# Kernel optimization log

Hardware: AMD Instinct MI355X
Metric: run time of the kernel (lower is better)

Reference implementation:

```python
import jax, jax.numpy as jnp
import numpy as np

N_NODES = 100000
N_EDGES = 1600000
MUL = 32            # channel multiplicity for every irrep
INV_SQRT_MUL = 1.0 / np.sqrt(32.0)
# path constants: wigner-3j norms (1/sqrt3 for 0x1->1 and 1x1->0, 1/sqrt6 for 1x1->1)
# combined with fan-in path normalization (fan=32 for 0e out, fan=64 for 1o out, 2 paths)
C_DOT = 1.0 / np.sqrt(3.0 * 32.0)
C_SCL = 1.0 / np.sqrt(3.0 * 64.0)
C_CRS = 1.0 / np.sqrt(6.0 * 64.0)


def setup_inputs() -> dict:
    key = jax.random.key(0)
    ks = jax.random.split(key, 12)
    x = jax.random.normal(ks[0], (N_NODES, 128), jnp.float32)
    pos = jax.random.normal(ks[1], (N_NODES, 3), jnp.float32)
    edge_index = jax.random.randint(ks[2], (2, N_EDGES), 0, N_NODES, jnp.int32)
    # o3.Linear(32x0e+32x1o -> 32x0e+32x0e+32x1o): per-irrep channel mixing
    W_node_s = jax.random.normal(ks[3], (32, 64), jnp.float32)   # 0e -> (scalars|gates)
    W_node_v = jax.random.normal(ks[4], (32, 32), jnp.float32)   # 1o -> 1o
    # FullyConnectedTensorProduct(32x0e+32x1o, 1x1o -> 32x0e+32x1o): 3 CG paths
    W_tp_d = jax.random.normal(ks[5], (32, 32), jnp.float32)     # 1o x 1o -> 0e (dot)
    W_tp_s = jax.random.normal(ks[6], (32, 32), jnp.float32)     # 0e x 1o -> 1o
    W_tp_c = jax.random.normal(ks[7], (32, 32), jnp.float32)     # 1o x 1o -> 1o (cross)
    # o3.Linear(32x0e+32x1o -> 32x0e+32x1o)
    W_msg_s = jax.random.normal(ks[8], (32, 32), jnp.float32)
    W_msg_v = jax.random.normal(ks[9], (32, 32), jnp.float32)
    ln_gamma = jnp.ones((128,), jnp.float32)
    ln_beta = jnp.zeros((128,), jnp.float32)
    return {"x": x, "pos": pos, "edge_index": edge_index,
            "W_node_s": W_node_s, "W_node_v": W_node_v,
            "W_tp_d": W_tp_d, "W_tp_s": W_tp_s, "W_tp_c": W_tp_c,
            "W_msg_s": W_msg_s, "W_msg_v": W_msg_v,
            "ln_gamma": ln_gamma, "ln_beta": ln_beta}


def reference(x, pos, edge_index, W_node_s, W_node_v, W_tp_d, W_tp_s, W_tp_c,
              W_msg_s, W_msg_v, ln_gamma, ln_beta):
    N = x.shape[0]
    row, col = edge_index[0], edge_index[1]
    # split node irreps: 32 scalars (0e) | 32 vectors (1o) of dim 3
    s = x[:, :32]                       # [N,32]
    v = x[:, 32:].reshape(-1, 32, 3)    # [N,32,3]
    # lin_node (equivariant linear, path-normalized by 1/sqrt(fan_in)=1/sqrt(32))
    h_s = (s @ W_node_s) * INV_SQRT_MUL                          # [N,64]
    h_v = jnp.einsum('nid,ij->njd', v, W_node_v) * INV_SQRT_MUL  # [N,32,3]
    # Gate: relu scalars, sigmoid gates multiply the gated vectors
    sc = jax.nn.relu(h_s[:, :32])                                # [N,32]
    hv = h_v * jax.nn.sigmoid(h_s[:, 32:])[:, :, None]           # [N,32,3]
    # spherical harmonics l=1, component norm: sqrt(3)*unit vec in e3nn (y,z,x) order
    rel = pos[col] - pos[row]                                    # [E,3]
    unit = rel / jnp.sqrt(jnp.sum(rel * rel, -1, keepdims=True) + 1e-12)
    u = jnp.sqrt(3.0) * unit[:, (1, 2, 0)]                       # [E,3]
    # gather source-node features per edge
    sj = sc[col]                                                 # [E,32]
    vj = hv[col]                                                 # [E,32,3]
    # CG tensor product paths
    dot = jnp.einsum('eid,ed->ei', vj, u)                        # 1o x 1o -> 0e
    crs = jnp.cross(vj, u[:, None, :])                           # 1o x 1o -> 1o
    m0 = (dot @ W_tp_d) * C_DOT                                  # [E,32]
    m1 = (sj @ W_tp_s)[:, :, None] * u[:, None, :] * C_SCL \
         + jnp.einsum('eid,ik->ekd', crs, W_tp_c) * C_CRS        # [E,32,3]
    m = jnp.concatenate([m0, m1.reshape(-1, 96)], -1)            # [E,128]
    # scatter-mean over destination nodes (row)
    deg = jax.ops.segment_sum(jnp.ones_like(row, jnp.float32), row,
                              num_segments=N).clip(1.0)
    mi = jax.ops.segment_sum(m, row, num_segments=N) / deg[:, None]
    # lin_msg
    ms = (mi[:, :32] @ W_msg_s) * INV_SQRT_MUL
    mv = jnp.einsum('nid,ij->njd', mi[:, 32:].reshape(-1, 32, 3),
                    W_msg_v) * INV_SQRT_MUL
    o = jnp.concatenate([ms, mv.reshape(-1, 96)], -1)            # [N,128]
    # LayerNorm over 128 dims (as in the original, affine)
    mu = o.mean(-1, keepdims=True)
    var = o.var(-1, keepdims=True)
    o = (o - mu) / jnp.sqrt(var + 1e-5) * ln_gamma + ln_beta
    return x + o
```

## Files before the change

### kernel.cpp

```cpp
#include <hip/hip_runtime.h>
#include <math.h>


static constexpr float INV_SQRT_MUL = 0.17677669529663687f;
static constexpr float C_DOT = 0.10206207261596575f;
static constexpr float C_SCL = 0.07216878364870322f;
static constexpr float C_CRS = 0.05103103630798288f;
static constexpr float SQRT3 = 1.7320508075688772f;
static constexpr int MAXDEG = 48;
static constexpr int SCAT_B = 2048;
static constexpr int CNT_WORDS = 8 * 16384;

#define WS_ALIGN(x) (((x) + 255) & ~(size_t)255)
#define CIDX(r) ((((r) & 7) << 14) | ((r) >> 3))

__device__ __forceinline__ unsigned short f2bf(float v) {
    unsigned int b = __float_as_uint(v);
    b += 0x7FFFu + ((b >> 16) & 1u);
    return (unsigned short)(b >> 16);
}
__device__ __forceinline__ float bf2f(unsigned short u) {
    return __uint_as_float(((unsigned int)u) << 16);
}

__global__ __launch_bounds__(1024)
void fuse_zero(const float* __restrict__ Wns, const float* __restrict__ Wnv,
               const float* __restrict__ Wtpd, const float* __restrict__ Wtps,
               const float* __restrict__ Wtpc, const float* __restrict__ Wms,
               const float* __restrict__ Wmv, float* __restrict__ Wall,
               int* __restrict__ cnt) {
    int t = threadIdx.x;
    if (blockIdx.x == 0) {
        int i = t >> 5, j = t & 31;
        float a = 0.f, b = 0.f, c = 0.f;
#pragma unroll
        for (int k = 0; k < 32; ++k) {
            a += Wtpd[i * 32 + k] * Wms[k * 32 + j];
            b += Wtps[i * 32 + k] * Wmv[k * 32 + j];
            c += Wtpc[i * 32 + k] * Wmv[k * 32 + j];
        }
        Wall[t]        = a * (C_DOT * INV_SQRT_MUL);
        Wall[1024 + t] = b * (C_SCL * INV_SQRT_MUL);
        Wall[2048 + t] = c * (C_CRS * INV_SQRT_MUL);
        int i2 = t >> 5, k2 = t & 31;
        Wall[3072 + t]        = Wns[k2 * 64 + i2];
        Wall[3072 + 1024 + t] = Wns[k2 * 64 + 32 + i2];
        Wall[5120 + t]        = Wnv[k2 * 32 + i2];
    } else {
        int i = (blockIdx.x - 1) * 1024 + t;
        if (i < CNT_WORDS) cnt[i] = 0;
    }
}

__global__ __launch_bounds__(256)
void scatter(const int* __restrict__ eidx, int* __restrict__ cnt,
             int* __restrict__ slots, int E) {
    int shard = blockIdx.x & 7;
    int tid = (blockIdx.x >> 3) * 256 + threadIdx.x;
    const int SSTRIDE = (SCAT_B / 8) * 256;
    int Q = E >> 2;
    const int4* r4p = (const int4*)eidx;
    const int4* c4p = (const int4*)(eidx + E);
    for (int q = tid; q < Q; q += SSTRIDE) {
        int4 R = r4p[q];
        bool any = ((R.x & 7) == shard) | ((R.y & 7) == shard) |
                   ((R.z & 7) == shard) | ((R.w & 7) == shard);
        if (!any) continue;
        int4 C = c4p[q];
        int rr[4] = {R.x, R.y, R.z, R.w};
        int cc[4] = {C.x, C.y, C.z, C.w};
#pragma unroll
        for (int k = 0; k < 4; ++k) {
            if ((rr[k] & 7) == shard) {
                int p = atomicAdd(&cnt[CIDX(rr[k])], 1);
                if (p < MAXDEG) slots[(size_t)rr[k] * MAXDEG + p] = cc[k];
            }
        }
    }
    for (int e = (Q << 2) + tid; e < E; e += SSTRIDE) {
        int r = eidx[e];
        if ((r & 7) == shard) {
            int c = eidx[E + e];
            int p = atomicAdd(&cnt[CIDX(r)], 1);
            if (p < MAXDEG) slots[(size_t)r * MAXDEG + p] = c;
        }
    }
}

__global__ __launch_bounds__(128)
void node_feat(const float* __restrict__ x, const float* __restrict__ WT,
               ushort4* __restrict__ feat4, int N) {
    __shared__ float buf[2][64 * 36];
    int t = threadIdx.x;
    int wv = t >> 6, l = t & 63;
    float* bw = buf[wv];
    int nt = (N + 63) >> 6;
    int tile = blockIdx.x * 2 + wv;
    if (tile >= nt) return;
    int B = tile << 6;
    int r0 = l >> 3, cw = (l & 7) << 2;
    const float* WnsT = WT;
    const float* WnvT = WT + 2048;

    auto stage = [&](int w0) {
#pragma unroll
        for (int j = 0; j < 8; ++j) {
            int row = j * 8 + r0;
            int node = B + row;
            float4 v = make_float4(0.f, 0.f, 0.f, 0.f);
            if (node < N) v = *(const float4*)(x + (size_t)node * 128 + w0 + cw);
            *(float4*)(bw + row * 36 + cw) = v;
        }
        __builtin_amdgcn_wave_barrier();
    };
    auto readrow = [&](float* dst) {
        const float4* rp = (const float4*)(bw + l * 36);
#pragma unroll
        for (int j = 0; j < 8; ++j) {
            float4 q = rp[j];
            dst[4*j] = q.x; dst[4*j+1] = q.y; dst[4*j+2] = q.z; dst[4*j+3] = q.w;
        }
        __builtin_amdgcn_wave_barrier();
    };

    float xs[32];
    stage(0); readrow(xs);
    unsigned int scp[16];
    float sig[32];
#pragma unroll 2
    for (int i = 0; i < 32; ++i) {
        float a = 0.f, g = 0.f;
#pragma unroll
        for (int k = 0; k < 32; ++k) {
            a += xs[k] * WnsT[i * 32 + k];
            g += xs[k] * WnsT[(32 + i) * 32 + k];
        }
        a = fmaxf(a * INV_SQRT_MUL, 0.f);
        float s = 1.f / (1.f + __expf(-g * INV_SQRT_MUL));
        unsigned short s16 = f2bf(a);
        if ((i & 1) == 0) scp[i >> 1] = s16;
        else scp[i >> 1] |= ((unsigned int)s16) << 16;
        sig[i] = s * INV_SQRT_MUL;
    }
    float xv[96];
    stage(32); readrow(xv);
    stage(64); readrow(xv + 32);
    stage(96); readrow(xv + 64);
    int node = B + l;
    bool liv = (node < N);
#pragma unroll 2
    for (int i = 0; i < 32; ++i) {
        float o0 = 0.f, o1 = 0.f, o2 = 0.f;
#pragma unroll
        for (int k = 0; k < 32; ++k) {
            float w = WnvT[i * 32 + k];
            o0 += xv[3 * k + 0] * w;
            o1 += xv[3 * k + 1] * w;
            o2 += xv[3 * k + 2] * w;
        }
        float s = sig[i];
        unsigned int scw = scp[i >> 1];
        ushort4 pk;
        pk.x = (unsigned short)((i & 1) ? (scw >> 16) : (scw & 0xFFFFu));
        pk.y = f2bf(o0 * s); pk.z = f2bf(o1 * s); pk.w = f2bf(o2 * s);
        if (liv) feat4[(size_t)node * 32 + i] = pk;
    }
}

__global__ __launch_bounds__(256)
void agg(const float* __restrict__ x, const float* __restrict__ pos,
         const ushort4* __restrict__ feat4, const int* __restrict__ cnt,
         const int* __restrict__ slots, const float* __restrict__ Wall,
         const float* __restrict__ gamma, const float* __restrict__ beta,
         float* __restrict__ out, int N) {
    __shared__ float4 cu[8][MAXDEG];
    __shared__ float4 finA[8][32];
    __shared__ float4 finB[8][32];
    int t = threadIdx.x;
    int hw = t >> 5, lane = t & 31;
    int n = blockIdx.x * 8 + hw;
    bool live = (n < N);
    int nn = live ? n : 0;

    int deg = cnt[CIDX(nn)];
    size_t srow = (size_t)nn * MAXDEG;
    int col0 = slots[srow + lane];
    int col1 = slots[srow + 32 + (lane & 15)];
    float prx = pos[nn * 3 + 0], pry = pos[nn * 3 + 1], prz = pos[nn * 3 + 2];
    if (!live) deg = 0;
    int c = min(deg, MAXDEG);
    int cpad = (c + 3) & ~3;

    if (lane < c) {
        float rx = pos[col0 * 3 + 0] - prx, ry = pos[col0 * 3 + 1] - pry, rz = pos[col0 * 3 + 2] - prz;
        float inv = rsqrtf(rx * rx + ry * ry + rz * rz + 1e-12f) * SQRT3;
        cu[hw][lane] = make_float4(ry * inv, rz * inv, rx * inv, __int_as_float(col0 << 8));
    } else {
        cu[hw][lane] = make_float4(0.f, 0.f, 0.f, __int_as_float(0));
    }
    if (lane < 16) {
        int idx = 32 + lane;
        if (idx < c) {
            float rx = pos[col1 * 3 + 0] - prx, ry = pos[col1 * 3 + 1] - pry, rz = pos[col1 * 3 + 2] - prz;
            float inv = rsqrtf(rx * rx + ry * ry + rz * rz + 1e-12f) * SQRT3;
            cu[hw][idx] = make_float4(ry * inv, rz * inv, rx * inv, __int_as_float(col1 << 8));
        } else {
            cu[hw][idx] = make_float4(0.f, 0.f, 0.f, __int_as_float(0));
        }
    }
    __builtin_amdgcn_wave_barrier();

    const char* featB = (const char*)feat4;
    unsigned int ch8 = (unsigned int)lane * 8u;
    const float4* cuw = cu[hw];
    float D = 0.f, S0 = 0.f, S1 = 0.f, S2 = 0.f, C0 = 0.f, C1 = 0.f, C2 = 0.f;

    for (int jb = 0; jb < cpad; jb += 4) {
        float4 q[4]; ushort4 f[4];
#pragma unroll
        for (int k = 0; k < 4; ++k) q[k] = cuw[jb + k];
#pragma unroll
        for (int k = 0; k < 4; ++k)
            f[k] = *(const ushort4*)(featB + (__float_as_uint(q[k].w) + ch8));
#pragma unroll
        for (int k = 0; k < 4; ++k) {
            float u0 = q[k].x, u1 = q[k].y, u2 = q[k].z;
            float sj = bf2f(f[k].x);
            float h0 = bf2f(f[k].y), h1 = bf2f(f[k].z), h2 = bf2f(f[k].w);
            D  += h0 * u0 + h1 * u1 + h2 * u2;
            S0 += sj * u0; S1 += sj * u1; S2 += sj * u2;
            C0 += h1 * u2 - h2 * u1;
            C1 += h2 * u0 - h0 * u2;
            C2 += h0 * u1 - h1 * u0;
        }
    }

    finA[hw][lane] = make_float4(D, S0, S1, S2);
    finB[hw][lane] = make_float4(C0, C1, C2, 0.f);
    __builtin_amdgcn_wave_barrier();

    float invdeg = 1.0f / (float)((deg > 0) ? deg : 1);
    float a0 = 0.f, aV0 = 0.f, aV1 = 0.f, aV2 = 0.f;
#pragma unroll 8
    for (int i = 0; i < 32; ++i) {
        float4 a = finA[hw][i];
        float4 b = finB[hw][i];
        float wd = Wall[i * 32 + lane];
        float ws = Wall[1024 + i * 32 + lane];
        float wc = Wall[2048 + i * 32 + lane];
        a0  += a.x * wd;
        aV0 += a.y * ws + b.x * wc;
        aV1 += a.z * ws + b.y * wc;
        aV2 += a.w * ws + b.z * wc;
    }
    float vd = a0 * invdeg;
    float v0 = aV0 * invdeg, v1 = aV1 * invdeg, v2 = aV2 * invdeg;

    float s1 = vd + v0 + v1 + v2;
    float s2 = vd * vd + v0 * v0 + v1 * v1 + v2 * v2;
#pragma unroll
    for (int m = 16; m >= 1; m >>= 1) {
        s1 += __shfl_xor(s1, m);
        s2 += __shfl_xor(s2, m);
    }
    float mu = s1 * (1.f / 128.f);
    float var = s2 * (1.f / 128.f) - mu * mu;
    float rstd = rsqrtf(var + 1e-5f);

    if (live) {
        size_t base = (size_t)n * 128;
        int chv = 32 + lane * 3;
        float xv0 = __builtin_nontemporal_load(&x[base + lane]);
        float xa  = __builtin_nontemporal_load(&x[base + chv + 0]);
        float xb  = __builtin_nontemporal_load(&x[base + chv + 1]);
        float xc  = __builtin_nontemporal_load(&x[base + chv + 2]);
        __builtin_nontemporal_store(xv0 + (vd - mu) * rstd * gamma[lane] + beta[lane], &out[base + lane]);
        __builtin_nontemporal_store(xa + (v0 - mu) * rstd * gamma[chv + 0] + beta[chv + 0], &out[base + chv + 0]);
        __builtin_nontemporal_store(xb + (v1 - mu) * rstd * gamma[chv + 1] + beta[chv + 1], &out[base + chv + 1]);
        __builtin_nontemporal_store(xc + (v2 - mu) * rstd * gamma[chv + 2] + beta[chv + 2], &out[base + chv + 2]);
    }
}

extern "C" void kernel_launch(void* const* d_in, const int* in_sizes, int n_in,
                              void* d_out, int out_size, void* d_ws, size_t ws_size,
                              hipStream_t stream) {
    const float* x     = (const float*)d_in[0];
    const float* pos   = (const float*)d_in[1];
    const int*   eidx  = (const int*)d_in[2];
    const float* Wns   = (const float*)d_in[3];
    const float* Wnv   = (const float*)d_in[4];
    const float* Wtpd  = (const float*)d_in[5];
    const float* Wtps  = (const float*)d_in[6];
    const float* Wtpc  = (const float*)d_in[7];
    const float* Wms   = (const float*)d_in[8];
    const float* Wmv   = (const float*)d_in[9];
    const float* gamma = (const float*)d_in[10];
    const float* beta  = (const float*)d_in[11];
    float* out = (float*)d_out;

    int N = in_sizes[0] / 128;
    int E = in_sizes[2] / 2;

    char* ws = (char*)d_ws;
    size_t off = 0;
    unsigned short* feat = (unsigned short*)(ws + off); off += WS_ALIGN((size_t)N * 128 * 2);
    int*   cnt  = (int*)(ws + off);   off += WS_ALIGN((size_t)CNT_WORDS * 4);
    float* Wall = (float*)(ws + off); off += WS_ALIGN(6144 * 4);
    int*   slots = (int*)(ws + off);

    int zb = 1 + (CNT_WORDS + 1023) / 1024;
    fuse_zero<<<zb, 1024, 0, stream>>>(Wns, Wnv, Wtpd, Wtps, Wtpc, Wms, Wmv, Wall, cnt);
    scatter<<<SCAT_B, 256, 0, stream>>>(eidx, cnt, slots, E);
    int nt = (N + 63) >> 6;
    node_feat<<<(nt + 1) / 2, 128, 0, stream>>>(x, Wall + 3072, (ushort4*)feat, N);
    agg<<<(N + 7) / 8, 256, 0, stream>>>(x, pos, (const ushort4*)feat, cnt, slots, Wall, gamma, beta, out, N);
}
```

Baseline: 352.3 us.

## Unroll edge gather by 8, vectorize transposed weight loads, nontemporal edge loads

Three separate tweaks are combined. The fused message weights are stored transposed so each lane can load its column as float4 vectors instead of 32 scalar strided loads. The neighbor gather loop is unrolled to 8 edges per step to put more independent feature loads in flight. The scatter pass reads edge indices with nontemporal loads to avoid polluting the cache. The wider unroll raises register pressure, and the float4 weight loads are per-lane strided, which may cost more than the previous coalesced scalar loads.

```diff
diff --git a/kernel.cpp b/kernel.cpp
--- a/kernel.cpp
+++ b/kernel.cpp
@@ -10,6 +10,8 @@
 static constexpr int MAXDEG = 48;
 static constexpr int SCAT_B = 2048;
 static constexpr int CNT_WORDS = 8 * 16384;
+
+typedef int vint4 __attribute__((ext_vector_type(4)));
 
 #define WS_ALIGN(x) (((x) + 255) & ~(size_t)255)
 #define CIDX(r) ((((r) & 7) << 14) | ((r) >> 3))
@@ -39,9 +41,9 @@
             b += Wtps[i * 32 + k] * Wmv[k * 32 + j];
             c += Wtpc[i * 32 + k] * Wmv[k * 32 + j];
         }
-        Wall[t]        = a * (C_DOT * INV_SQRT_MUL);
-        Wall[1024 + t] = b * (C_SCL * INV_SQRT_MUL);
-        Wall[2048 + t] = c * (C_CRS * INV_SQRT_MUL);
+        Wall[j * 32 + i]        = a * (C_DOT * INV_SQRT_MUL);
+        Wall[1024 + j * 32 + i] = b * (C_SCL * INV_SQRT_MUL);
+        Wall[2048 + j * 32 + i] = c * (C_CRS * INV_SQRT_MUL);
         int i2 = t >> 5, k2 = t & 31;
         Wall[3072 + t]        = Wns[k2 * 64 + i2];
         Wall[3072 + 1024 + t] = Wns[k2 * 64 + 32 + i2];
@@ -59,14 +61,14 @@
     int tid = (blockIdx.x >> 3) * 256 + threadIdx.x;
     const int SSTRIDE = (SCAT_B / 8) * 256;
     int Q = E >> 2;
-    const int4* r4p = (const int4*)eidx;
-    const int4* c4p = (const int4*)(eidx + E);
+    const vint4* r4p = (const vint4*)eidx;
+    const vint4* c4p = (const vint4*)(eidx + E);
     for (int q = tid; q < Q; q += SSTRIDE) {
-        int4 R = r4p[q];
+        vint4 R = __builtin_nontemporal_load(&r4p[q]);
         bool any = ((R.x & 7) == shard) | ((R.y & 7) == shard) |
                    ((R.z & 7) == shard) | ((R.w & 7) == shard);
         if (!any) continue;
-        int4 C = c4p[q];
+        vint4 C = __builtin_nontemporal_load(&c4p[q]);
         int rr[4] = {R.x, R.y, R.z, R.w};
         int cc[4] = {C.x, C.y, C.z, C.w};
 #pragma unroll
@@ -215,7 +217,29 @@
     const float4* cuw = cu[hw];
     float D = 0.f, S0 = 0.f, S1 = 0.f, S2 = 0.f, C0 = 0.f, C1 = 0.f, C2 = 0.f;
 
-    for (int jb = 0; jb < cpad; jb += 4) {
+    auto body = [&](const float4& q, const ushort4& f) {
+        float u0 = q.x, u1 = q.y, u2 = q.z;
+        float sj = bf2f(f.x);
+        float h0 = bf2f(f.y), h1 = bf2f(f.z), h2 = bf2f(f.w);
+        D  += h0 * u0 + h1 * u1 + h2 * u2;
+        S0 += sj * u0; S1 += sj * u1; S2 += sj * u2;
+        C0 += h1 * u2 - h2 * u1;
+        C1 += h2 * u0 - h0 * u2;
+        C2 += h0 * u1 - h1 * u0;
+    };
+
+    int jb = 0;
+    for (; jb + 8 <= cpad; jb += 8) {
+        float4 q[8]; ushort4 f[8];
+#pragma unroll
+        for (int k = 0; k < 8; ++k) q[k] = cuw[jb + k];
+#pragma unroll
+        for (int k = 0; k < 8; ++k)
+            f[k] = *(const ushort4*)(featB + (__float_as_uint(q[k].w) + ch8));
+#pragma unroll
+        for (int k = 0; k < 8; ++k) body(q[k], f[k]);
+    }
+    if (jb < cpad) {
         float4 q[4]; ushort4 f[4];
 #pragma unroll
         for (int k = 0; k < 4; ++k) q[k] = cuw[jb + k];
@@ -223,16 +247,7 @@
         for (int k = 0; k < 4; ++k)
             f[k] = *(const ushort4*)(featB + (__float_as_uint(q[k].w) + ch8));
 #pragma unroll
-        for (int k = 0; k < 4; ++k) {
-            float u0 = q[k].x, u1 = q[k].y, u2 = q[k].z;
-            float sj = bf2f(f[k].x);
-            float h0 = bf2f(f[k].y), h1 = bf2f(f[k].z), h2 = bf2f(f[k].w);
-            D  += h0 * u0 + h1 * u1 + h2 * u2;
-            S0 += sj * u0; S1 += sj * u1; S2 += sj * u2;
-            C0 += h1 * u2 - h2 * u1;
-            C1 += h2 * u0 - h0 * u2;
-            C2 += h0 * u1 - h1 * u0;
-        }
+        for (int k = 0; k < 4; ++k) body(q[k], f[k]);
     }
 
     finA[hw][lane] = make_float4(D, S0, S1, S2);
@@ -241,17 +256,25 @@
 
     float invdeg = 1.0f / (float)((deg > 0) ? deg : 1);
     float a0 = 0.f, aV0 = 0.f, aV1 = 0.f, aV2 = 0.f;
-#pragma unroll 8
-    for (int i = 0; i < 32; ++i) {
-        float4 a = finA[hw][i];
-        float4 b = finB[hw][i];
-        float wd = Wall[i * 32 + lane];
-        float ws = Wall[1024 + i * 32 + lane];
-        float wc = Wall[2048 + i * 32 + lane];
-        a0  += a.x * wd;
-        aV0 += a.y * ws + b.x * wc;
-        aV1 += a.z * ws + b.y * wc;
-        aV2 += a.w * ws + b.z * wc;
+    const float4* W4 = (const float4*)Wall;
+#pragma unroll
+    for (int c4 = 0; c4 < 8; ++c4) {
+        float4 wd4 = W4[lane * 8 + c4];
+        float4 ws4 = W4[256 + lane * 8 + c4];
+        float4 wc4 = W4[512 + lane * 8 + c4];
+        float wdv[4] = {wd4.x, wd4.y, wd4.z, wd4.w};
+        float wsv[4] = {ws4.x, ws4.y, ws4.z, ws4.w};
+        float wcv[4] = {wc4.x, wc4.y, wc4.z, wc4.w};
+#pragma unroll
+        for (int m = 0; m < 4; ++m) {
+            int i = c4 * 4 + m;
+            float4 a = finA[hw][i];
+            float4 b = finB[hw][i];
+            a0  += a.x * wdv[m];
+            aV0 += a.y * wsv[m] + b.x * wcv[m];
+            aV1 += a.z * wsv[m] + b.y * wcv[m];
+            aV2 += a.w * wsv[m] + b.z * wcv[m];
+        }
     }
     float vd = a0 * invdeg;
     float v0 = aV0 * invdeg, v1 = aV1 * invdeg, v2 = aV2 * invdeg;
```

Measured after the change: 434.7 us. 1.23x slower.
